# Kernel optimization log

Measured on AMD Instinct MI355X. Metric: run time of the kernel, lower is better.

## Reference

```python
import jax, jax.numpy as jnp
import numpy as np

D_MODEL = 512
NHEAD = 8
SEQ = 2048
BATCH = 4


def setup_inputs() -> dict:
    key = jax.random.key(0)
    ks = jax.random.split(key, 6)
    s = 0.02
    return {
        "x": jax.random.normal(ks[0], (SEQ, BATCH, D_MODEL), jnp.float32),
        "w_in_g": jax.random.normal(ks[1], (3 * D_MODEL, D_MODEL), jnp.float32) * s,
        "b_in_g": jnp.zeros((3 * D_MODEL,), jnp.float32),
        "w_out_g": jax.random.normal(ks[2], (D_MODEL, D_MODEL), jnp.float32) * s,
        "b_out_g": jnp.zeros((D_MODEL,), jnp.float32),
        "w_in_l": jax.random.normal(ks[3], (3 * D_MODEL, D_MODEL), jnp.float32) * s,
        "b_in_l": jnp.zeros((3 * D_MODEL,), jnp.float32),
        "w_out_l": jax.random.normal(ks[4], (D_MODEL, D_MODEL), jnp.float32) * s,
        "b_out_l": jnp.zeros((D_MODEL,), jnp.float32),
        "local_window_size": 128,
    }


def _mha(x, w_in, b_in, w_out, b_out, nhead):
    # x: (S, B, D); faithful to torch nn.MultiheadAttention (batch_first=False)
    S, B, D = x.shape
    dh = D // nhead
    qkv = x @ w_in.T + b_in                       # (S, B, 3D)
    q, k, v = jnp.split(qkv, 3, axis=-1)
    q = q.reshape(S, B, nhead, dh)
    k = k.reshape(S, B, nhead, dh)
    v = v.reshape(S, B, nhead, dh)
    scores = jnp.einsum("sbhd,tbhd->bhst", q, k) / jnp.sqrt(jnp.float32(dh))
    attn = jax.nn.softmax(scores, axis=-1)        # (B, H, S, S)
    out = jnp.einsum("bhst,tbhd->sbhd", attn, v).reshape(S, B, D)
    return out @ w_out.T + b_out


def reference(x, w_in_g, b_in_g, w_out_g, b_out_g,
              w_in_l, b_in_l, w_out_l, b_out_l, local_window_size):
    S, B, D = x.shape
    W = int(local_window_size)
    global_out = _mha(x, w_in_g, b_in_g, w_out_g, b_out_g, NHEAD)
    # Non-overlapping local windows tile the sequence (S % W == 0 here),
    # so the per-window loop == window-batched attention.
    nW = S // W
    xw = x.reshape(nW, W, B, D).transpose(1, 0, 2, 3).reshape(W, nW * B, D)
    lw = _mha(xw, w_in_l, b_in_l, w_out_l, b_out_l, NHEAD)
    local_out = lw.reshape(W, nW, B, D).transpose(1, 0, 2, 3).reshape(S, B, D)
    return global_out + local_out
```

## Files before the change

kernel.cpp:

```cpp
#include <hip/hip_runtime.h>
#include <hip/hip_bf16.h>
#include <stdint.h>

typedef __attribute__((ext_vector_type(8))) short bf16x8;
typedef __attribute__((ext_vector_type(8))) unsigned short u16x8;
typedef __attribute__((ext_vector_type(4))) float f32x4;

#define DEV __device__ __forceinline__

DEV f32x4 mfma16(bf16x8 a, bf16x8 b, f32x4 c) {
  return __builtin_amdgcn_mfma_f32_16x16x32_bf16(a, b, c, 0, 0, 0);
}

DEV void gload_lds16(const void* g, void* l) {
  __builtin_amdgcn_global_load_lds(
      (__attribute__((address_space(1))) void*)(g),
      (__attribute__((address_space(3))) void*)(l), 16, 0, 0);
}

DEV unsigned short f2bf(float f) {
  __hip_bfloat16 h = __float2bfloat16(f);
  return __builtin_bit_cast(unsigned short, h);
}

__global__ __launch_bounds__(256) void convert_all(
    const float4* __restrict__ s0, const float4* __restrict__ s1,
    const float4* __restrict__ s2, const float4* __restrict__ s3,
    const float4* __restrict__ s4, ushort4* __restrict__ dst)
{
  const int n0 = 1048576, n1 = 196608, n3 = 65536;
  int i = blockIdx.x * 256 + threadIdx.x;
  const float4* s; int off;
  if (i < n0)                 { s = s0; off = 0; }
  else if (i < n0 + n1)       { s = s1; off = n0; }
  else if (i < n0 + 2*n1)     { s = s2; off = n0 + n1; }
  else if (i < n0 + 2*n1+n3)  { s = s3; off = n0 + 2*n1; }
  else                        { s = s4; off = n0 + 2*n1 + n3; }
  float4 v = s[i - off];
  ushort4 o;
  o.x = f2bf(v.x); o.y = f2bf(v.y); o.z = f2bf(v.z); o.w = f2bf(v.w);
  dst[i] = o;
}

#define GEMM_STAGE(Ap, Wp, k0v, bufi)                                          \
  {                                                                            \
    _Pragma("unroll")                                                          \
    for (int is = 0; is < 2; ++is) {                                           \
      const int row = is*64 + (t >> 3);                                        \
      const int slot = (t & 7) ^ (row & 7);                                    \
      gload_lds16((Ap) + (long)(m0 + row)*K + (k0v) + slot*8,                  \
                  (char*)&As[bufi][0] + (is*512 + t)*16);                      \
      gload_lds16((Wp) + (long)(n0 + row)*K + (k0v) + slot*8,                  \
                  (char*)&Ws[bufi][0] + (is*512 + t)*16);                      \
    }                                                                          \
  }

#define GEMM_COMPUTE(cur, NJ, WCMUL)                                           \
  {                                                                            \
    const char* Apl = (const char*)&As[cur][0];                                \
    const char* Wpl = (const char*)&Ws[cur][0];                                \
    __builtin_amdgcn_s_setprio(1);                                             \
    _Pragma("unroll")                                                          \
    for (int kk = 0; kk < 2; ++kk) {                                           \
      bf16x8 af[4], wf[NJ];                                                    \
      _Pragma("unroll")                                                        \
      for (int i = 0; i < 4; ++i) {                                            \
        const int row = wr*64 + i*16 + l16;                                    \
        const int slot = (kk*4 + g16) ^ (row & 7);                             \
        af[i] = *(const bf16x8*)(Apl + row*128 + slot*16);                     \
      }                                                                        \
      _Pragma("unroll")                                                        \
      for (int j = 0; j < NJ; ++j) {                                           \
        const int row = wc*WCMUL + j*16 + l16;                                 \
        const int slot = (kk*4 + g16) ^ (row & 7);                             \
        wf[j] = *(const bf16x8*)(Wpl + row*128 + slot*16);                     \
      }                                                                        \
      _Pragma("unroll")                                                        \
      for (int i = 0; i < 4; ++i)                                              \
        _Pragma("unroll")                                                      \
        for (int j = 0; j < NJ; ++j)                                           \
          acc[i][j] = mfma16(af[i], wf[j], acc[i][j]);                         \
    }                                                                          \
    __builtin_amdgcn_s_setprio(0);                                             \
  }

__global__ __launch_bounds__(512) void gemm_qkv(
    const __hip_bfloat16* __restrict__ A0,
    const __hip_bfloat16* __restrict__ Wg, const float* __restrict__ bg,
    const __hip_bfloat16* __restrict__ Wl, const float* __restrict__ bl,
    __hip_bfloat16* __restrict__ qkg, __hip_bfloat16* __restrict__ vtg,
    __hip_bfloat16* __restrict__ qkl, __hip_bfloat16* __restrict__ vtl,
    int M, int N, int K)
{
  __shared__ __attribute__((aligned(16))) char SMEM[65536];
  __hip_bfloat16 (*As)[8192] = (__hip_bfloat16(*)[8192])SMEM;
  __hip_bfloat16 (*Ws)[8192] = (__hip_bfloat16(*)[8192])(SMEM + 32768);
  const int t = threadIdx.x;
  const int lane = t & 63, wid = t >> 6;
  const int g16 = lane >> 4, l16 = lane & 15;
  const int wr = wid >> 2, wc = wid & 3;
  const int bid = blockIdx.x;
  const int xcd = bid & 7, seq = bid >> 3;
  const int sel = xcd >= 4;
  const int xh = xcd & 3;
  const int m0 = (xh*16 + (seq & 15)) * 128;
  const int n0 = (seq >> 4) * 128;
  const __hip_bfloat16* W0 = sel ? Wl : Wg;
  const float* b0 = sel ? bl : bg;
  __hip_bfloat16* qkp = sel ? qkl : qkg;
  __hip_bfloat16* vtp = sel ? vtl : vtg;

  f32x4 acc[4][2] = {};
  const int nks = K >> 6;

  GEMM_STAGE(A0, W0, 0, 0)
  for (int step = 0; step < nks; ++step) {
    const int cur = step & 1;
    if (step + 1 < nks) {
      GEMM_STAGE(A0, W0, (step+1) << 6, cur ^ 1)
      asm volatile("s_waitcnt vmcnt(4)" ::: "memory");
    } else {
      asm volatile("s_waitcnt vmcnt(0)" ::: "memory");
    }
    __builtin_amdgcn_s_barrier();
    asm volatile("" ::: "memory");
    GEMM_COMPUTE(cur, 2, 32)
    asm volatile("" ::: "memory");
    __builtin_amdgcn_s_barrier();
  }

  if (n0 < 1024) {
#pragma unroll
    for (int i = 0; i < 4; ++i) {
      const int gr = m0 + wr*64 + i*16 + g16*4;
#pragma unroll
      for (int j = 0; j < 2; ++j) {
        const int gc = n0 + wc*32 + j*16 + l16;
        const float bias = b0[gc];
        const float scl = (gc >= 512) ? 0.180336880f : 1.0f;
#pragma unroll
        for (int r = 0; r < 4; ++r)
          qkp[(long)(gr + r)*1024 + gc] =
              __float2bfloat16((acc[i][j][r] + bias) * scl);
      }
    }
  } else {
    const int n0l = n0 - 1024;
    short* T = (short*)SMEM;
#pragma unroll
    for (int i = 0; i < 4; ++i) {
      const int sl = wr*16 + i*4 + g16;
#pragma unroll
      for (int j = 0; j < 2; ++j) {
        const int gcl = wc*32 + j*16 + l16;
        const float bias = b0[n0 + gcl];
#pragma unroll
        for (int r = 0; r < 4; ++r)
          T[gcl*136 + r*32 + sl] = (short)f2bf(acc[i][j][r] + bias);
      }
    }
    __syncthreads();
    const int d = t & 127, b4 = t >> 7;
    __hip_bfloat16* dst = vtp + ((long)(b4*512 + n0l + d))*2048 + (m0 >> 2);
#pragma unroll
    for (int k = 0; k < 4; ++k) {
      u16x8 v = *(const u16x8*)(T + d*136 + b4*32 + k*8);
      *(u16x8*)(dst + k*8) = v;
    }
  }
}

__global__ __launch_bounds__(512) void gemm_out(
    const __hip_bfloat16* __restrict__ A0, const __hip_bfloat16* __restrict__ W0,
    const float* __restrict__ b0,
    const __hip_bfloat16* __restrict__ A1, const __hip_bfloat16* __restrict__ W1,
    const float* __restrict__ b1,
    float* __restrict__ Cout, int M, int N, int K)
{
  __shared__ __attribute__((aligned(16))) __hip_bfloat16 As[2][128*64];
  __shared__ __attribute__((aligned(16))) __hip_bfloat16 Ws[2][64*64];
  const int t = threadIdx.x;
  const int lane = t & 63, wid = t >> 6;
  const int g16 = lane >> 4, l16 = lane & 15;
  const int wr = wid >> 2, wc = wid & 3;
  const int bid = blockIdx.x;
  const int xcd = bid & 7, pos = bid >> 3;
  const int m0 = (xcd*8 + (pos & 7)) * 128, n0 = (pos >> 3) * 64;

  f32x4 acc[4][1] = {};
  const int nks = K >> 6;
  const int NS = 2*nks;

#define OUT_STAGE(Ap, Wp, k0v, bufi)                                           \
  {                                                                            \
    _Pragma("unroll")                                                          \
    for (int is = 0; is < 2; ++is) {                                           \
      const int row = is*64 + (t >> 3);                                        \
      const int slot = (t & 7) ^ (row & 7);                                    \
      gload_lds16((Ap) + (long)(m0 + row)*K + (k0v) + slot*8,                  \
                  (char*)&As[bufi][0] + (is*512 + t)*16);                      \
    }                                                                          \
    {                                                                          \
      const int row = t >> 3;                                                  \
      const int slot = (t & 7) ^ (row & 7);                                    \
      gload_lds16((Wp) + (long)(n0 + row)*K + (k0v) + slot*8,                  \
                  (char*)&Ws[bufi][0] + t*16);                                 \
    }                                                                          \
  }

  OUT_STAGE(A0, W0, 0, 0)
  for (int step = 0; step < NS; ++step) {
    const int cur = step & 1;
    if (step + 1 < NS) {
      const int nstep = step + 1;
      const __hip_bfloat16* Ap = (nstep >= nks) ? A1 : A0;
      const __hip_bfloat16* Wp = (nstep >= nks) ? W1 : W0;
      const int k0 = ((nstep >= nks) ? (nstep - nks) : nstep) << 6;
      OUT_STAGE(Ap, Wp, k0, cur ^ 1)
      asm volatile("s_waitcnt vmcnt(3)" ::: "memory");
    } else {
      asm volatile("s_waitcnt vmcnt(0)" ::: "memory");
    }
    __builtin_amdgcn_s_barrier();
    asm volatile("" ::: "memory");
    GEMM_COMPUTE(cur, 1, 16)
    asm volatile("" ::: "memory");
    __builtin_amdgcn_s_barrier();
  }

#pragma unroll
  for (int i = 0; i < 4; ++i) {
    const int gr = m0 + wr*64 + i*16 + g16*4;
    const int gc = n0 + wc*16 + l16;
    const float bias = b0[gc] + b1[gc];
#pragma unroll
    for (int r = 0; r < 4; ++r)
      Cout[(long)(gr + r)*N + gc] = acc[i][0][r] + bias;
  }
}

__global__ __launch_bounds__(512) void flash_all(
    const __hip_bfloat16* __restrict__ qkg, const __hip_bfloat16* __restrict__ vtg,
    __hip_bfloat16* __restrict__ outg,
    const __hip_bfloat16* __restrict__ qkl, const __hip_bfloat16* __restrict__ vtl,
    __hip_bfloat16* __restrict__ outl,
    const int* __restrict__ wptr, int S, int B, int blkoff)
{
  const int t = threadIdx.x, lane = t & 63, w = t >> 6;
  const int g16 = lane >> 4, l16 = lane & 15;
  const int gid = blockIdx.x + blkoff;
  const int isl = gid >= 512;
  const int id = gid & 511;
  const __hip_bfloat16* qk = isl ? qkl : qkg;
  const __hip_bfloat16* vt = isl ? vtl : vtg;
  __hip_bfloat16* outb = isl ? outl : outg;
  const int Wn = isl ? wptr[0] : S;
  const int xcd = id & 7, seq = id >> 3;
  const int bh = xcd + 8*(seq & 3);
  const int qt = seq >> 2;
  const int b = bh >> 3, h = bh & 7;
  const int q0 = qt * 128;
  const int kv0 = (q0 / Wn) * Wn;
  const int nkt = Wn >> 6;
  const int vtb = bh * 64;

  __shared__ __attribute__((aligned(16))) __hip_bfloat16 Kb[2][64*64];
  __shared__ __attribute__((aligned(16))) __hip_bfloat16 Vb[2][64*64];
  __shared__ __attribute__((aligned(16))) short Pl[8][16*72];

  const int qrow = q0 + w*16 + l16;
  bf16x8 qa[2];
  {
    const __hip_bfloat16* qp = qk + ((long)qrow*B + b)*1024 + h*64 + g16*8;
    qa[0] = *(const bf16x8*)(const void*)qp;
    qa[1] = *(const bf16x8*)(const void*)(qp + 32);
  }
  bf16x8 aones;
#pragma unroll
  for (int e = 0; e < 8; ++e) aones[e] = (short)0x3F80;

  f32x4 o[4] = {};
  f32x4 ol = {};

#define STAGE(tile, bufi)                                                      \
  {                                                                            \
    const int kvs_ = kv0 + (tile)*64;                                          \
    const int row_ = t >> 3;                                                   \
    const int sl_ = (t & 7) ^ (row_ & 7);                                      \
    gload_lds16(qk + ((long)(kvs_+row_)*B + b)*1024 + 512 + h*64 + sl_*8,      \
                (char*)&Kb[bufi][0] + t*16);                                   \
    gload_lds16(vt + (long)(vtb + row_)*2048 + kvs_ + sl_*8,                   \
                (char*)&Vb[bufi][0] + t*16);                                   \
  }

  STAGE(0, 0)

  for (int kt = 0; kt < nkt; ++kt) {
    const int cur = kt & 1;
    if (kt + 1 < nkt) {
      STAGE(kt + 1, cur ^ 1)
      asm volatile("s_waitcnt vmcnt(2)" ::: "memory");
    } else {
      asm volatile("s_waitcnt vmcnt(0)" ::: "memory");
    }
    __builtin_amdgcn_s_barrier();
    asm volatile("" ::: "memory");

    f32x4 s[4] = {};
    const char* Kp = (const char*)&Kb[cur][0];
    __builtin_amdgcn_s_setprio(1);
#pragma unroll
    for (int kk = 0; kk < 2; ++kk)
#pragma unroll
      for (int j = 0; j < 4; ++j) {
        const int row = j*16 + l16;
        const int slot = (kk*4 + g16) ^ (row & 7);
        bf16x8 kf = *(const bf16x8*)(Kp + row*128 + slot*16);
        s[j] = mfma16(kf, qa[kk], s[j]);
      }
    __builtin_amdgcn_s_setprio(0);

    short* Pw = &Pl[w][0];
#pragma unroll
    for (int j = 0; j < 4; ++j) {
      short4 pk4;
      pk4.x = (short)f2bf(__builtin_amdgcn_exp2f(s[j][0]));
      pk4.y = (short)f2bf(__builtin_amdgcn_exp2f(s[j][1]));
      pk4.z = (short)f2bf(__builtin_amdgcn_exp2f(s[j][2]));
      pk4.w = (short)f2bf(__builtin_amdgcn_exp2f(s[j][3]));
      *(short4*)(Pw + l16*72 + j*16 + g16*4) = pk4;
    }

    __builtin_amdgcn_s_setprio(1);
#pragma unroll
    for (int kk = 0; kk < 2; ++kk) {
      bf16x8 pf = *(const bf16x8*)(Pw + l16*72 + kk*32 + g16*8);
      ol = mfma16(aones, pf, ol);
#pragma unroll
      for (int dblk = 0; dblk < 4; ++dblk) {
        const int row = dblk*16 + l16;
        const int slot = (kk*4 + g16) ^ (row & 7);
        bf16x8 vf = *(const bf16x8*)((const char*)&Vb[cur][0] + row*128 + slot*16);
        o[dblk] = mfma16(vf, pf, o[dblk]);
      }
    }
    __builtin_amdgcn_s_setprio(0);

    asm volatile("" ::: "memory");
    __builtin_amdgcn_s_barrier();
  }

  const float inv = 1.f / ol[0];
  const long obase = ((long)qrow*B + b)*512 + h*64;
#pragma unroll
  for (int dblk = 0; dblk < 4; ++dblk) {
    ushort4 pk;
    pk.x = f2bf(o[dblk][0]*inv); pk.y = f2bf(o[dblk][1]*inv);
    pk.z = f2bf(o[dblk][2]*inv); pk.w = f2bf(o[dblk][3]*inv);
    *(ushort4*)(outb + obase + dblk*16 + g16*4) = pk;
  }
}

extern "C" void kernel_launch(void* const* d_in, const int* in_sizes, int n_in,
                              void* d_out, int out_size, void* d_ws, size_t ws_size,
                              hipStream_t stream) {
  const float* x   = (const float*)d_in[0];
  const float* wig = (const float*)d_in[1];
  const float* big = (const float*)d_in[2];
  const float* wog = (const float*)d_in[3];
  const float* bog = (const float*)d_in[4];
  const float* wil = (const float*)d_in[5];
  const float* bil = (const float*)d_in[6];
  const float* wol = (const float*)d_in[7];
  const float* bol = (const float*)d_in[8];
  const int*   wsz = (const int*)d_in[9];

  char* ws = (char*)d_ws;
  __hip_bfloat16* xb    = (__hip_bfloat16*)(ws + 0);
  __hip_bfloat16* wigb  = (__hip_bfloat16*)(ws + 8388608);
  __hip_bfloat16* wilb  = (__hip_bfloat16*)(ws + 9961472);
  __hip_bfloat16* wogb  = (__hip_bfloat16*)(ws + 11534336);
  __hip_bfloat16* wolb  = (__hip_bfloat16*)(ws + 12058624);
  __hip_bfloat16* qkg   = (__hip_bfloat16*)(ws + 12582912);
  __hip_bfloat16* qkl   = (__hip_bfloat16*)(ws + 29360128);
  __hip_bfloat16* vtg   = (__hip_bfloat16*)(ws + 46137344);
  __hip_bfloat16* vtl   = (__hip_bfloat16*)(ws + 54525952);
  __hip_bfloat16* attng = xb;

  const int big_ws = ws_size >= (size_t)71303168;
  __hip_bfloat16* attnl = big_ws ? (__hip_bfloat16*)(ws + 62914560)
                                 : qkg;

  convert_all<<<6144, 256, 0, stream>>>(
      (const float4*)x, (const float4*)wig, (const float4*)wil,
      (const float4*)wog, (const float4*)wol, (ushort4*)ws);

  gemm_qkv<<<1536, 512, 0, stream>>>(xb, wigb, big, wilb, bil,
                                     qkg, vtg, qkl, vtl, 8192, 1536, 512);

  if (big_ws) {
    flash_all<<<1024, 512, 0, stream>>>(qkg, vtg, attng, qkl, vtl, attnl,
                                        wsz, 2048, 4, 0);
  } else {
    flash_all<<<512, 512, 0, stream>>>(qkg, vtg, attng, qkl, vtl, attnl,
                                       wsz, 2048, 4, 0);
    flash_all<<<512, 512, 0, stream>>>(qkg, vtg, attng, qkl, vtl, attnl,
                                       wsz, 2048, 4, 512);
  }

  gemm_out<<<512, 512, 0, stream>>>(attng, wogb, bog, attnl, wolb, bol,
                                    (float*)d_out, 8192, 512, 512);
}
```

Baseline: 111.5 us.

## Add 32x32-MFMA global flash kernel with 256-row query tiles

Adds a dedicated global-attention kernel in which each block handles 256 query rows, one 32-row strip per wave. It uses 32x32x16 bf16 MFMA for both QK^T and PV, double-buffers K/V tiles into LDS, and uses permlane32 swaps to turn the P accumulators into operands for the PV MFMA. The aim is to halve K/V refetch per query and get more work out of each MFMA instruction. The generic flash_all kernel now handles only the local windows, in a separate launch. This removes the single fused launch, so global and local attention no longer overlap and the large-workspace path disappears.

After: 127.4 us. 14.3% more time.

```diff
diff --git a/kernel.cpp b/kernel.cpp
--- a/kernel.cpp
+++ b/kernel.cpp
@@ -5,11 +5,16 @@
 typedef __attribute__((ext_vector_type(8))) short bf16x8;
 typedef __attribute__((ext_vector_type(8))) unsigned short u16x8;
 typedef __attribute__((ext_vector_type(4))) float f32x4;
+typedef __attribute__((ext_vector_type(16))) float f32x16;
 
 #define DEV __device__ __forceinline__
 
 DEV f32x4 mfma16(bf16x8 a, bf16x8 b, f32x4 c) {
   return __builtin_amdgcn_mfma_f32_16x16x32_bf16(a, b, c, 0, 0, 0);
+}
+
+DEV f32x16 mfma32(bf16x8 a, bf16x8 b, f32x16 c) {
+  return __builtin_amdgcn_mfma_f32_32x32x16_bf16(a, b, c, 0, 0, 0);
 }
 
 DEV void gload_lds16(const void* g, void* l) {
@@ -239,6 +244,129 @@
   }
 }
 
+__global__ __launch_bounds__(512) void flash_g256(
+    const __hip_bfloat16* __restrict__ qk, const __hip_bfloat16* __restrict__ vt,
+    __hip_bfloat16* __restrict__ outg, int S, int B)
+{
+  const int t = threadIdx.x, lane = t & 63, w = t >> 6;
+  const int l32 = lane & 31, hf = lane >> 5;
+  const int id = blockIdx.x;
+  const int xcd = id & 7, seq = id >> 3;
+  const int bh = xcd + 8*(seq & 3);
+  const int qt = seq >> 2;
+  const int b = bh >> 3, head = bh & 7;
+  const int q0 = qt * 256;
+  const int nkt = S >> 6;
+  const int vtb = bh * 64;
+
+  __shared__ __attribute__((aligned(16))) __hip_bfloat16 Kb[2][64*64];
+  __shared__ __attribute__((aligned(16))) __hip_bfloat16 Vb[2][64*64];
+
+  const int qw = q0 + w*32 + l32;
+  bf16x8 qa[4];
+  {
+    const __hip_bfloat16* qp = qk + ((long)qw*B + b)*1024 + head*64 + hf*8;
+#pragma unroll
+    for (int ks = 0; ks < 4; ++ks)
+      qa[ks] = *(const bf16x8*)(const void*)(qp + ks*16);
+  }
+
+  f32x16 oacc[2] = {};
+  float lsum = 0.f;
+
+#define GSTAGE(tile, bufi)                                                     \
+  {                                                                            \
+    const int kvs_ = (tile)*64;                                                \
+    const int row_ = t >> 3;                                                   \
+    const int sl_ = (t & 7) ^ (row_ & 7);                                      \
+    gload_lds16(qk + ((long)(kvs_+row_)*B + b)*1024 + 512 + head*64 + sl_*8,   \
+                (char*)&Kb[bufi][0] + t*16);                                   \
+    gload_lds16(vt + (long)(vtb + row_)*2048 + kvs_ + sl_*8,                   \
+                (char*)&Vb[bufi][0] + t*16);                                   \
+  }
+
+  GSTAGE(0, 0)
+
+  for (int kt = 0; kt < nkt; ++kt) {
+    const int cur = kt & 1;
+    if (kt + 1 < nkt) {
+      GSTAGE(kt + 1, cur ^ 1)
+      asm volatile("s_waitcnt vmcnt(2)" ::: "memory");
+    } else {
+      asm volatile("s_waitcnt vmcnt(0)" ::: "memory");
+    }
+    __builtin_amdgcn_s_barrier();
+    asm volatile("" ::: "memory");
+
+    f32x16 sacc[2] = {};
+    const char* Kp = (const char*)&Kb[cur][0];
+    __builtin_amdgcn_s_setprio(1);
+#pragma unroll
+    for (int ks = 0; ks < 4; ++ks)
+#pragma unroll
+      for (int jb = 0; jb < 2; ++jb) {
+        const int row = jb*32 + l32;
+        const int slot = (ks*2 + hf) ^ (row & 7);
+        bf16x8 kf = *(const bf16x8*)(Kp + row*128 + slot*16);
+        sacc[jb] = mfma32(kf, qa[ks], sacc[jb]);
+      }
+    __builtin_amdgcn_s_setprio(0);
+
+    unsigned pk[2][8];
+#pragma unroll
+    for (int jb = 0; jb < 2; ++jb)
+#pragma unroll
+      for (int rg = 0; rg < 4; ++rg)
+#pragma unroll
+        for (int hv = 0; hv < 2; ++hv) {
+          const float p0 = __builtin_amdgcn_exp2f(sacc[jb][rg*4 + hv*2]);
+          const float p1 = __builtin_amdgcn_exp2f(sacc[jb][rg*4 + hv*2 + 1]);
+          lsum += p0 + p1;
+          pk[jb][rg*2 + hv] =
+              (unsigned)f2bf(p0) | ((unsigned)f2bf(p1) << 16);
+        }
+
+    const char* Vp = (const char*)&Vb[cur][0];
+    __builtin_amdgcn_s_setprio(1);
+#pragma unroll
+    for (int ks = 0; ks < 4; ++ks) {
+      const int q2 = ks & 1, jb = ks >> 1;
+      unsigned w0 = pk[jb][4*q2 + 0], w2v = pk[jb][4*q2 + 2];
+      asm volatile("v_permlane32_swap_b32 %0, %1" : "+v"(w0), "+v"(w2v));
+      unsigned w1 = pk[jb][4*q2 + 1], w3v = pk[jb][4*q2 + 3];
+      asm volatile("v_permlane32_swap_b32 %0, %1" : "+v"(w1), "+v"(w3v));
+      union { unsigned u[4]; bf16x8 v; } pb;
+      pb.u[0] = w0; pb.u[1] = w1; pb.u[2] = w2v; pb.u[3] = w3v;
+#pragma unroll
+      for (int db = 0; db < 2; ++db) {
+        const int row = db*32 + l32;
+        const int slot = (ks*2 + hf) ^ (row & 7);
+        bf16x8 vf = *(const bf16x8*)(Vp + row*128 + slot*16);
+        oacc[db] = mfma32(vf, pb.v, oacc[db]);
+      }
+    }
+    __builtin_amdgcn_s_setprio(0);
+
+    asm volatile("" ::: "memory");
+    __builtin_amdgcn_s_barrier();
+  }
+
+  lsum += __shfl_xor(lsum, 32, 64);
+  const float inv = 1.f / lsum;
+  const long base = ((long)qw*B + b)*512 + head*64;
+#pragma unroll
+  for (int db = 0; db < 2; ++db)
+#pragma unroll
+    for (int rq = 0; rq < 4; ++rq) {
+      ushort4 pkk;
+      pkk.x = f2bf(oacc[db][rq*4 + 0]*inv);
+      pkk.y = f2bf(oacc[db][rq*4 + 1]*inv);
+      pkk.z = f2bf(oacc[db][rq*4 + 2]*inv);
+      pkk.w = f2bf(oacc[db][rq*4 + 3]*inv);
+      *(ushort4*)(outg + base + db*32 + rq*8 + hf*4) = pkk;
+    }
+}
+
 __global__ __launch_bounds__(512) void flash_all(
     const __hip_bfloat16* __restrict__ qkg, const __hip_bfloat16* __restrict__ vtg,
     __hip_bfloat16* __restrict__ outg,
@@ -390,7 +518,6 @@
   const int big_ws = ws_size >= (size_t)71303168;
   __hip_bfloat16* attnl = big_ws ? (__hip_bfloat16*)(ws + 62914560)
                                  : qkg;
-
   convert_all<<<6144, 256, 0, stream>>>(
       (const float4*)x, (const float4*)wig, (const float4*)wil,
       (const float4*)wog, (const float4*)wol, (ushort4*)ws);
@@ -398,15 +525,9 @@
   gemm_qkv<<<1536, 512, 0, stream>>>(xb, wigb, big, wilb, bil,
                                      qkg, vtg, qkl, vtl, 8192, 1536, 512);
 
-  if (big_ws) {
-    flash_all<<<1024, 512, 0, stream>>>(qkg, vtg, attng, qkl, vtl, attnl,
-                                        wsz, 2048, 4, 0);
-  } else {
-    flash_all<<<512, 512, 0, stream>>>(qkg, vtg, attng, qkl, vtl, attnl,
-                                       wsz, 2048, 4, 0);
-    flash_all<<<512, 512, 0, stream>>>(qkg, vtg, attng, qkl, vtl, attnl,
-                                       wsz, 2048, 4, 512);
-  }
+  flash_g256<<<256, 512, 0, stream>>>(qkg, vtg, attng, 2048, 4);
+  flash_all<<<512, 512, 0, stream>>>(qkg, vtg, attng, qkl, vtl, attnl,
+                                     wsz, 2048, 4, 512);
 
   gemm_out<<<512, 512, 0, stream>>>(attng, wogb, bog, attnl, wolb, bol,
                                     (float*)d_out, 8192, 512, 512);
```
